# Optimization experiments

Measured on AMD Instinct MI355X. Metric: run time of the kernel, lower is better.

Reference implementation:

```python
import jax, jax.numpy as jnp
import numpy as np

EPS = 1e-6
ROPE_BASE = 10000.0
N_HEADS = 16
N_KV_HEADS = 4
NUM_EXPERTS = 8
TOP_K = 2


def rms_norm(x, w):
    rms = jax.lax.rsqrt(jnp.mean(x * x, axis=-1, keepdims=True) + EPS)
    return x * rms * w


def rope_tables(seq_len, head_dim):
    inv_freq = 1.0 / ROPE_BASE ** (jnp.arange(0, head_dim, 2, dtype=jnp.float32) / head_dim)
    t = jnp.arange(seq_len, dtype=jnp.float32)
    freqs = jnp.outer(t, inv_freq)              # [S, D/2]
    emb = jnp.concatenate([freqs, freqs], -1)    # [S, D]
    return jnp.cos(emb), jnp.sin(emb)


def apply_rotary(x, cos, sin):
    # x: [B, S, H, D]; cos/sin: [S, D]
    c = cos[None, :, None, 0::2]
    s = sin[None, :, None, 0::2]
    x1 = x[..., 0::2]
    x2 = x[..., 1::2]
    y1 = x1 * c - x2 * s
    y2 = x1 * s + x2 * c
    return jnp.stack([y1, y2], axis=-1).reshape(x.shape)


def attention(x, wq, wk, wv, wo):
    B, S, D = x.shape
    hd = D // N_HEADS
    q = (x @ wq.T).reshape(B, S, N_HEADS, hd)
    k = (x @ wk.T).reshape(B, S, N_KV_HEADS, hd)
    v = (x @ wv.T).reshape(B, S, N_KV_HEADS, hd)
    cos, sin = rope_tables(S, hd)
    q = apply_rotary(q, cos, sin)
    k = apply_rotary(k, cos, sin)
    n_rep = N_HEADS // N_KV_HEADS
    k = jnp.repeat(k, n_rep, axis=2)
    v = jnp.repeat(v, n_rep, axis=2)
    q = q.transpose(0, 2, 1, 3)  # [B,H,S,D]
    k = k.transpose(0, 2, 1, 3)
    v = v.transpose(0, 2, 1, 3)
    scores = jnp.einsum('bhqd,bhkd->bhqk', q, k) / jnp.sqrt(jnp.float32(hd))
    causal = jnp.tril(jnp.ones((S, S), dtype=bool))
    scores = jnp.where(causal[None, None], scores, jnp.finfo(scores.dtype).min)
    attn = jax.nn.softmax(scores, axis=-1)
    out = jnp.einsum('bhqk,bhkd->bhqd', attn, v)
    out = out.transpose(0, 2, 1, 3).reshape(B, S, D)
    return out @ wo.T


def moe(x, router_w, Wg, Wu, Wd):
    B, S, D = x.shape
    logits = x @ router_w.T                       # [B,S,E]
    probs = jax.nn.softmax(logits, axis=-1)
    topk_probs, topk_idx = jax.lax.top_k(probs, TOP_K)
    topk_probs = topk_probs / jnp.sum(topk_probs, axis=-1, keepdims=True)
    one_hot = jax.nn.one_hot(topk_idx, NUM_EXPERTS, dtype=jnp.float32)  # [B,S,K,E]
    tokens_per_expert = jnp.sum(one_hot, axis=(0, 1, 2))                # [E]
    f = tokens_per_expert / jnp.sum(tokens_per_expert)
    P = jnp.mean(probs.reshape(-1, NUM_EXPERTS), axis=0)
    aux_loss = NUM_EXPERTS * jnp.sum(f * P)
    # Dense all-expert SwiGLU then gather-combine (same math as masked dispatch)
    g = jnp.einsum('bsd,efd->bsef', x, Wg)        # [B,S,E,F]
    u = jnp.einsum('bsd,efd->bsef', x, Wu)
    h = jax.nn.silu(g) * u
    y = jnp.einsum('bsef,edf->bsed', h, Wd)       # [B,S,E,D]
    idx = jnp.broadcast_to(topk_idx[..., None], (B, S, TOP_K, D))
    sel = jnp.take_along_axis(y, idx, axis=2)     # [B,S,K,D]
    out = jnp.sum(topk_probs[..., None] * sel, axis=2)
    return out, aux_loss, tokens_per_expert


def setup_inputs() -> dict:
    key = jax.random.key(0)
    ks = jax.random.split(key, 9)
    d_model, d_ff, E = 1024, 2048, NUM_EXPERTS
    sc = 0.02
    return {
        'x': jax.random.normal(ks[0], (2, 2048, d_model), jnp.float32),
        'wq': jax.random.normal(ks[1], (d_model, d_model), jnp.float32) * sc,
        'wk': jax.random.normal(ks[2], (256, d_model), jnp.float32) * sc,
        'wv': jax.random.normal(ks[3], (256, d_model), jnp.float32) * sc,
        'wo': jax.random.normal(ks[4], (d_model, d_model), jnp.float32) * sc,
        'attn_norm_w': jnp.ones((d_model,), jnp.float32),
        'ffn_norm_w': jnp.ones((d_model,), jnp.float32),
        'router_w': jax.random.normal(ks[5], (E, d_model), jnp.float32) * sc,
        'Wg': jax.random.normal(ks[6], (E, d_ff, d_model), jnp.float32) * sc,
        'Wu': jax.random.normal(ks[7], (E, d_ff, d_model), jnp.float32) * sc,
        'Wd': jax.random.normal(ks[8], (E, d_model, d_ff), jnp.float32) * sc,
    }


def reference(x, wq, wk, wv, wo, attn_norm_w, ffn_norm_w, router_w, Wg, Wu, Wd):
    x = x + attention(rms_norm(x, attn_norm_w), wq, wk, wv, wo)
    moe_out, aux_loss, tokens_per_expert = moe(rms_norm(x, ffn_norm_w), router_w, Wg, Wu, Wd)
    x = x + moe_out
    return (x, aux_loss, tokens_per_expert)
```

## Files before the change

kernel.cpp:

```cpp
#include <hip/hip_runtime.h>
#include <hip/hip_bf16.h>
#include <math.h>

typedef __attribute__((ext_vector_type(4))) float f32x4;
typedef __attribute__((ext_vector_type(8))) short bf16x8;
typedef __attribute__((ext_vector_type(8))) unsigned short u16x8;

#define D_MODEL 1024
#define DFF 2048
#define S_LEN 2048
#define T_TOK 4096
#define NEXP 8

__device__ __forceinline__ unsigned short f2bf(float f){
  union { float f; unsigned u; } v; v.f = f;
  unsigned u = v.u;
  u += 0x7fffu + ((u >> 16) & 1u);
  return (unsigned short)(u >> 16);
}

__global__ __launch_bounds__(256) void k_rmsnorm(const float* __restrict__ x,
    const float* __restrict__ w, float* __restrict__ out){
  const int t = blockIdx.x;
  const int tid = threadIdx.x;
  const float* row = x + (size_t)t * D_MODEL;
  float4 v = *(const float4*)(row + tid * 4);
  float ss = v.x*v.x + v.y*v.y + v.z*v.z + v.w*v.w;
  #pragma unroll
  for (int m = 1; m < 64; m <<= 1) ss += __shfl_xor(ss, m);
  __shared__ float red[4];
  if ((tid & 63) == 0) red[tid >> 6] = ss;
  __syncthreads();
  float tot = red[0] + red[1] + red[2] + red[3];
  float mean = tot * (1.0f / D_MODEL);
  float r = (float)(1.0 / sqrt((double)mean + 1e-6));
  float4 wv = *(const float4*)(w + tid * 4);
  float4 o;
  o.x = v.x * r * wv.x; o.y = v.y * r * wv.y;
  o.z = v.z * r * wv.z; o.w = v.w * r * wv.w;
  *(float4*)(out + (size_t)t * D_MODEL + tid * 4) = o;
}

__global__ __launch_bounds__(256) void k_gemm_f32(
    const float* __restrict__ A, int lda,
    const float* __restrict__ B0, const float* __restrict__ B1, const float* __restrict__ B2,
    int nb1, int nb2,
    float* __restrict__ C, int ldc,
    const float* __restrict__ resid, int K)
{
  __shared__ float As[16][132];
  __shared__ float Bs[16][132];
  const int n0 = blockIdx.x * 128, m0 = blockIdx.y * 128;
  const float* Bp; int nsub;
  if (B2 && n0 >= nb2)      { Bp = B2; nsub = n0 - nb2; }
  else if (B1 && n0 >= nb1) { Bp = B1; nsub = n0 - nb1; }
  else                      { Bp = B0; nsub = n0; }
  const int tid = threadIdx.x;
  const int sr = tid >> 1, sc = (tid & 1) << 3;
  const float* ap = A + (size_t)(m0 + sr) * lda + sc;
  const float* bp = Bp + (size_t)(nsub + sr) * K + sc;
  float acc[8][8];
  #pragma unroll
  for (int i = 0; i < 8; i++)
    #pragma unroll
    for (int j = 0; j < 8; j++) acc[i][j] = 0.f;
  const int tm = (tid >> 4) << 3, tn = (tid & 15) << 3;
  for (int k0 = 0; k0 < K; k0 += 16){
    float4 a0 = *(const float4*)(ap + k0);
    float4 a1 = *(const float4*)(ap + k0 + 4);
    float4 b0 = *(const float4*)(bp + k0);
    float4 b1 = *(const float4*)(bp + k0 + 4);
    As[sc+0][sr] = a0.x; As[sc+1][sr] = a0.y; As[sc+2][sr] = a0.z; As[sc+3][sr] = a0.w;
    As[sc+4][sr] = a1.x; As[sc+5][sr] = a1.y; As[sc+6][sr] = a1.z; As[sc+7][sr] = a1.w;
    Bs[sc+0][sr] = b0.x; Bs[sc+1][sr] = b0.y; Bs[sc+2][sr] = b0.z; Bs[sc+3][sr] = b0.w;
    Bs[sc+4][sr] = b1.x; Bs[sc+5][sr] = b1.y; Bs[sc+6][sr] = b1.z; Bs[sc+7][sr] = b1.w;
    __syncthreads();
    #pragma unroll
    for (int kk = 0; kk < 16; kk++){
      float a[8], b[8];
      *(float4*)(a)     = *(const float4*)&As[kk][tm];
      *(float4*)(a + 4) = *(const float4*)&As[kk][tm + 4];
      *(float4*)(b)     = *(const float4*)&Bs[kk][tn];
      *(float4*)(b + 4) = *(const float4*)&Bs[kk][tn + 4];
      #pragma unroll
      for (int i = 0; i < 8; i++)
        #pragma unroll
        for (int j = 0; j < 8; j++) acc[i][j] = fmaf(a[i], b[j], acc[i][j]);
    }
    __syncthreads();
  }
  #pragma unroll
  for (int i = 0; i < 8; i++){
    int row = m0 + tm + i;
    float* cp = C + (size_t)row * ldc + n0 + tn;
    if (resid){
      const float* rp = resid + (size_t)row * ldc + n0 + tn;
      #pragma unroll
      for (int j = 0; j < 8; j++) cp[j] = acc[i][j] + rp[j];
    } else {
      float4 v0, v1;
      v0.x = acc[i][0]; v0.y = acc[i][1]; v0.z = acc[i][2]; v0.w = acc[i][3];
      v1.x = acc[i][4]; v1.y = acc[i][5]; v1.z = acc[i][6]; v1.w = acc[i][7];
      *(float4*)cp = v0; *(float4*)(cp + 4) = v1;
    }
  }
}

__global__ void k_rope_table(float* __restrict__ ctab, float* __restrict__ stab){
  int idx = blockIdx.x * 256 + threadIdx.x;
  int pos = idx >> 4, kx = idx & 15;
  double inv = 1.0 / pow(10000.0, (double)kx / 16.0);
  float invf = (float)inv;
  float ang = (float)pos * invf;
  ctab[idx] = (float)cos((double)ang);
  stab[idx] = (float)sin((double)ang);
}

__global__ __launch_bounds__(256) void k_rope(float* __restrict__ qkv,
    const float* __restrict__ ctab, const float* __restrict__ stab){
  int idx = blockIdx.x * 256 + threadIdx.x;
  int t = idx / 640, p = idx - t * 640;
  int col, ph;
  if (p < 512){ int h = p >> 5; ph = p & 31; col = h * 64 + 2 * ph; }
  else { int p2 = p - 512; int h = p2 >> 5; ph = p2 & 31; col = 1024 + h * 64 + 2 * ph; }
  int pos = t & (S_LEN - 1);
  float c = ctab[pos * 16 + (ph & 15)];
  float s = stab[pos * 16 + (ph & 15)];
  float* base = qkv + (size_t)t * 1536 + col;
  float x1 = base[0], x2 = base[1];
  base[0] = x1 * c - x2 * s;
  base[1] = x1 * s + x2 * c;
}

__global__ __launch_bounds__(64) void k_attn(float* __restrict__ qkv){
  const int bx = blockIdx.x;
  const int h  = blockIdx.y;
  const int b  = blockIdx.z;
  const int tid = threadIdx.x;
  const int tok = b * S_LEN + bx * 64 + tid;
  __shared__ float Ks[64][68];
  __shared__ float Vs[64][68];
  float q[64], O[64];
  {
    const float* qp = qkv + (size_t)tok * 1536 + h * 64;
    #pragma unroll
    for (int c = 0; c < 16; c++){
      float4 v = *(const float4*)(qp + c * 4);
      q[c*4+0] = v.x * 0.125f; q[c*4+1] = v.y * 0.125f;
      q[c*4+2] = v.z * 0.125f; q[c*4+3] = v.w * 0.125f;
    }
  }
  #pragma unroll
  for (int d = 0; d < 64; d++) O[d] = 0.f;
  float m = -INFINITY, l = 0.f;
  const int kvh = h >> 2;
  const float* kbase = qkv + (size_t)(b * S_LEN) * 1536 + 1024 + kvh * 64;
  const float* vbase = kbase + 256;
  for (int kt = 0; kt <= bx; ++kt){
    #pragma unroll
    for (int i = 0; i < 16; i++){
      int r = i * 4 + (tid >> 4);
      int c = (tid & 15) << 2;
      size_t grow = (size_t)(kt * 64 + r) * 1536;
      *(float4*)&Ks[r][c] = *(const float4*)(kbase + grow + c);
      *(float4*)&Vs[r][c] = *(const float4*)(vbase + grow + c);
    }
    __syncthreads();
    const int jmax = (kt == bx) ? tid : 63;
    #pragma unroll
    for (int ch = 0; ch < 2; ++ch){
      const int jb = ch * 32;
      float s[32];
      #pragma unroll
      for (int jj = 0; jj < 32; jj += 2){
        float s0 = 0.f, s1 = 0.f;
        const float* kr0 = &Ks[jb + jj][0];
        const float* kr1 = &Ks[jb + jj + 1][0];
        #pragma unroll
        for (int c = 0; c < 16; c++){
          float4 k0 = *(const float4*)(kr0 + c * 4);
          float4 k1 = *(const float4*)(kr1 + c * 4);
          s0 = fmaf(q[c*4+0], k0.x, s0); s0 = fmaf(q[c*4+1], k0.y, s0);
          s0 = fmaf(q[c*4+2], k0.z, s0); s0 = fmaf(q[c*4+3], k0.w, s0);
          s1 = fmaf(q[c*4+0], k1.x, s1); s1 = fmaf(q[c*4+1], k1.y, s1);
          s1 = fmaf(q[c*4+2], k1.z, s1); s1 = fmaf(q[c*4+3], k1.w, s1);
        }
        s[jj] = s0; s[jj + 1] = s1;
      }
      float tmax = -INFINITY;
      #pragma unroll
      for (int jj = 0; jj < 32; jj++)
        if (jb + jj <= jmax) tmax = fmaxf(tmax, s[jj]);
      float mn = fmaxf(m, tmax);
      float corr = expf(m - mn);
      l *= corr;
      #pragma unroll
      for (int d = 0; d < 64; d++) O[d] *= corr;
      float ps = 0.f;
      #pragma unroll
      for (int jj = 0; jj < 32; jj++){
        float p = (jb + jj <= jmax) ? expf(s[jj] - mn) : 0.f;
        s[jj] = p; ps += p;
      }
      l += ps;
      #pragma unroll
      for (int jj = 0; jj < 32; jj++){
        float p = s[jj];
        const float* vr = &Vs[jb + jj][0];
        #pragma unroll
        for (int c = 0; c < 16; c++){
          float4 v4 = *(const float4*)(vr + c * 4);
          O[c*4+0] = fmaf(p, v4.x, O[c*4+0]);
          O[c*4+1] = fmaf(p, v4.y, O[c*4+1]);
          O[c*4+2] = fmaf(p, v4.z, O[c*4+2]);
          O[c*4+3] = fmaf(p, v4.w, O[c*4+3]);
        }
      }
      m = mn;
    }
    __syncthreads();
  }
  float inv_l = 1.f / l;
  float* op = qkv + (size_t)tok * 1536 + h * 64;
  #pragma unroll
  for (int c = 0; c < 16; c++){
    float4 o4;
    o4.x = O[c*4+0] * inv_l; o4.y = O[c*4+1] * inv_l;
    o4.z = O[c*4+2] * inv_l; o4.w = O[c*4+3] * inv_l;
    *(float4*)(op + c * 4) = o4;
  }
}

__global__ __launch_bounds__(64) void k_router(const float* __restrict__ norm2,
    const float* __restrict__ rw, float* __restrict__ p_all,
    int2* __restrict__ idx2, float2* __restrict__ tokw){
  const int t = blockIdx.x;
  const int lane = threadIdx.x;
  const float* xr = norm2 + (size_t)t * D_MODEL;
  float part[8];
  #pragma unroll
  for (int e = 0; e < 8; e++) part[e] = 0.f;
  #pragma unroll
  for (int c = 0; c < 4; c++){
    float4 xv = *(const float4*)(xr + c * 256 + lane * 4);
    #pragma unroll
    for (int e = 0; e < 8; e++){
      float4 wv = *(const float4*)(rw + e * D_MODEL + c * 256 + lane * 4);
      part[e] += xv.x*wv.x + xv.y*wv.y + xv.z*wv.z + xv.w*wv.w;
    }
  }
  #pragma unroll
  for (int e = 0; e < 8; e++){
    float v = part[e];
    #pragma unroll
    for (int msk = 1; msk < 64; msk <<= 1) v += __shfl_xor(v, msk);
    part[e] = v;
  }
  if (lane == 0){
    float mx = part[0];
    #pragma unroll
    for (int e = 1; e < 8; e++) mx = fmaxf(mx, part[e]);
    float p[8]; float sum = 0.f;
    #pragma unroll
    for (int e = 0; e < 8; e++){ p[e] = expf(part[e] - mx); sum += p[e]; }
    float inv = 1.f / sum;
    #pragma unroll
    for (int e = 0; e < 8; e++) p[e] *= inv;
    int i1 = 0;
    for (int e = 1; e < 8; e++) if (p[e] > p[i1]) i1 = e;
    int i2 = (i1 == 0) ? 1 : 0;
    for (int e = 0; e < 8; e++){ if (e != i1 && p[e] > p[i2]) i2 = e; }
    float denom = p[i1] + p[i2];
    float2 w; w.x = p[i1] / denom; w.y = p[i2] / denom;
    #pragma unroll
    for (int e = 0; e < 8; e++) p_all[t * 8 + e] = p[e];
    idx2[t] = make_int2(i1, i2);
    tokw[t] = w;
  }
}

__global__ __launch_bounds__(256) void k_finalize(const float* __restrict__ p_all,
    const int2* __restrict__ idx2, float* __restrict__ out,
    int* __restrict__ cnt, int* __restrict__ offs, int* __restrict__ cursor){
  __shared__ int sc[8];
  __shared__ float sp[8];
  const int tid = threadIdx.x;
  if (tid < 8){ sc[tid] = 0; sp[tid] = 0.f; }
  __syncthreads();
  int cl[8]; float pl[8];
  #pragma unroll
  for (int e = 0; e < 8; e++){ cl[e] = 0; pl[e] = 0.f; }
  for (int t = tid; t < T_TOK; t += 256){
    int2 id = idx2[t];
    cl[id.x]++; cl[id.y]++;
    #pragma unroll
    for (int e = 0; e < 8; e++) pl[e] += p_all[t * 8 + e];
  }
  #pragma unroll
  for (int e = 0; e < 8; e++){ atomicAdd(&sc[e], cl[e]); atomicAdd(&sp[e], pl[e]); }
  __syncthreads();
  if (tid == 0){
    float aux = 0.f; int off = 0;
    for (int e = 0; e < 8; e++){
      out[4194305 + e] = (float)sc[e];
      aux += ((float)sc[e] / 8192.0f) * (sp[e] / 4096.0f);
      offs[e] = off; cnt[e] = sc[e]; cursor[e] = 0; off += sc[e];
    }
    out[4194304] = aux * 8.0f;
  }
}

__global__ __launch_bounds__(256) void k_scatter(const int2* __restrict__ idx2,
    const float2* __restrict__ tokw, const int* __restrict__ offs,
    int* __restrict__ cursor, int* __restrict__ perm, float* __restrict__ wgt){
  int t = blockIdx.x * 256 + threadIdx.x;
  if (t >= T_TOK) return;
  int2 id = idx2[t]; float2 w = tokw[t];
  int p1 = atomicAdd(&cursor[id.x], 1);
  perm[offs[id.x] + p1] = t; wgt[offs[id.x] + p1] = w.x;
  int p2 = atomicAdd(&cursor[id.y], 1);
  perm[offs[id.y] + p2] = t; wgt[offs[id.y] + p2] = w.y;
}

__global__ __launch_bounds__(256) void k_moe_a(
    const float* __restrict__ norm2, const float* __restrict__ Wg, const float* __restrict__ Wu,
    const int* __restrict__ cnt, const int* __restrict__ offs,
    const int* __restrict__ perm, unsigned short* __restrict__ Hbuf)
{
  int rem = blockIdx.x, e = -1, m0 = 0;
  #pragma unroll
  for (int i = 0; i < 8; i++){
    int nt = (cnt[i] + 63) >> 6;
    if (e < 0 && rem < nt){ e = i; m0 = rem << 6; }
    if (e < 0) rem -= nt;
  }
  if (e < 0) return;
  const int n0 = blockIdx.y * 128;
  const int ne = cnt[e];
  const int seg0 = offs[e];
  __shared__ unsigned short As[64][40];
  __shared__ unsigned short Bg[128][40];
  __shared__ unsigned short Bu[128][40];
  const int tid = threadIdx.x;
  const int lane = tid & 63, w = tid >> 6;
  const int wm = w >> 1, wn = w & 1;
  f32x4 accg[2][4], accu[2][4];
  #pragma unroll
  for (int i = 0; i < 2; i++)
    #pragma unroll
    for (int j = 0; j < 4; j++){
      accg[i][j] = (f32x4){0.f,0.f,0.f,0.f};
      accu[i][j] = (f32x4){0.f,0.f,0.f,0.f};
    }
  const int ar = tid >> 1, ah = (tid & 1) << 4;
  bool aval = false; const float* asrc = norm2;
  if (tid < 128){
    aval = (m0 + ar < ne);
    int token = aval ? perm[seg0 + m0 + ar] : 0;
    asrc = norm2 + (size_t)token * D_MODEL + ah;
  }
  const int br = tid & 127;
  const float* bsrc = ((tid >> 7) ? Wu : Wg) + (size_t)e * DFF * D_MODEL
                      + (size_t)(n0 + br) * D_MODEL;
  unsigned short (*Bt)[40] = (tid >> 7) ? Bu : Bg;
  const int fr = lane & 15, fk = (lane >> 4) << 3;
  for (int k0 = 0; k0 < D_MODEL; k0 += 32){
    if (tid < 128){
      u16x8 w0 = (u16x8){0,0,0,0,0,0,0,0}, w1 = w0;
      if (aval){
        float4 f0 = *(const float4*)(asrc + k0);
        float4 f1 = *(const float4*)(asrc + k0 + 4);
        float4 f2 = *(const float4*)(asrc + k0 + 8);
        float4 f3 = *(const float4*)(asrc + k0 + 12);
        w0[0]=f2bf(f0.x); w0[1]=f2bf(f0.y); w0[2]=f2bf(f0.z); w0[3]=f2bf(f0.w);
        w0[4]=f2bf(f1.x); w0[5]=f2bf(f1.y); w0[6]=f2bf(f1.z); w0[7]=f2bf(f1.w);
        w1[0]=f2bf(f2.x); w1[1]=f2bf(f2.y); w1[2]=f2bf(f2.z); w1[3]=f2bf(f2.w);
        w1[4]=f2bf(f3.x); w1[5]=f2bf(f3.y); w1[6]=f2bf(f3.z); w1[7]=f2bf(f3.w);
      }
      *(u16x8*)&As[ar][ah] = w0;
      *(u16x8*)&As[ar][ah + 8] = w1;
    }
    {
      float4 f0 = *(const float4*)(bsrc + k0);
      float4 f1 = *(const float4*)(bsrc + k0 + 4);
      float4 f2 = *(const float4*)(bsrc + k0 + 8);
      float4 f3 = *(const float4*)(bsrc + k0 + 12);
      float4 f4 = *(const float4*)(bsrc + k0 + 16);
      float4 f5 = *(const float4*)(bsrc + k0 + 20);
      float4 f6 = *(const float4*)(bsrc + k0 + 24);
      float4 f7 = *(const float4*)(bsrc + k0 + 28);
      u16x8 w0, w1, w2, w3;
      w0[0]=f2bf(f0.x); w0[1]=f2bf(f0.y); w0[2]=f2bf(f0.z); w0[3]=f2bf(f0.w);
      w0[4]=f2bf(f1.x); w0[5]=f2bf(f1.y); w0[6]=f2bf(f1.z); w0[7]=f2bf(f1.w);
      w1[0]=f2bf(f2.x); w1[1]=f2bf(f2.y); w1[2]=f2bf(f2.z); w1[3]=f2bf(f2.w);
      w1[4]=f2bf(f3.x); w1[5]=f2bf(f3.y); w1[6]=f2bf(f3.z); w1[7]=f2bf(f3.w);
      w2[0]=f2bf(f4.x); w2[1]=f2bf(f4.y); w2[2]=f2bf(f4.z); w2[3]=f2bf(f4.w);
      w2[4]=f2bf(f5.x); w2[5]=f2bf(f5.y); w2[6]=f2bf(f5.z); w2[7]=f2bf(f5.w);
      w3[0]=f2bf(f6.x); w3[1]=f2bf(f6.y); w3[2]=f2bf(f6.z); w3[3]=f2bf(f6.w);
      w3[4]=f2bf(f7.x); w3[5]=f2bf(f7.y); w3[6]=f2bf(f7.z); w3[7]=f2bf(f7.w);
      *(u16x8*)&Bt[br][0]  = w0; *(u16x8*)&Bt[br][8]  = w1;
      *(u16x8*)&Bt[br][16] = w2; *(u16x8*)&Bt[br][24] = w3;
    }
    __syncthreads();
    bf16x8 af0 = *(const bf16x8*)&As[wm*32 + fr][fk];
    bf16x8 af1 = *(const bf16x8*)&As[wm*32 + 16 + fr][fk];
    #pragma unroll
    for (int fn = 0; fn < 4; fn++){
      bf16x8 bg = *(const bf16x8*)&Bg[wn*64 + fn*16 + fr][fk];
      bf16x8 bu = *(const bf16x8*)&Bu[wn*64 + fn*16 + fr][fk];
      accg[0][fn] = __builtin_amdgcn_mfma_f32_16x16x32_bf16(af0, bg, accg[0][fn], 0, 0, 0);
      accg[1][fn] = __builtin_amdgcn_mfma_f32_16x16x32_bf16(af1, bg, accg[1][fn], 0, 0, 0);
      accu[0][fn] = __builtin_amdgcn_mfma_f32_16x16x32_bf16(af0, bu, accu[0][fn], 0, 0, 0);
      accu[1][fn] = __builtin_amdgcn_mfma_f32_16x16x32_bf16(af1, bu, accu[1][fn], 0, 0, 0);
    }
    __syncthreads();
  }
  const int r0 = (lane >> 4) << 2, cix = lane & 15;
  #pragma unroll
  for (int fm = 0; fm < 2; fm++)
    #pragma unroll
    for (int fn = 0; fn < 4; fn++)
      #pragma unroll
      for (int reg = 0; reg < 4; reg++){
        int ml = wm*32 + fm*16 + r0 + reg;
        if (m0 + ml < ne){
          int nl = wn*64 + fn*16 + cix;
          float g = accg[fm][fn][reg];
          float u = accu[fm][fn][reg];
          float h = g / (1.f + __expf(-g)) * u;
          Hbuf[(size_t)(seg0 + m0 + ml) * DFF + n0 + nl] = f2bf(h);
        }
      }
}

__global__ __launch_bounds__(256) void k_moe_b(
    const unsigned short* __restrict__ Hbuf, const float* __restrict__ Wd,
    const int* __restrict__ cnt, const int* __restrict__ offs,
    const int* __restrict__ perm, const float* __restrict__ wgt,
    float* __restrict__ outx)
{
  int rem = blockIdx.x, e = -1, m0 = 0;
  #pragma unroll
  for (int i = 0; i < 8; i++){
    int nt = (cnt[i] + 63) >> 6;
    if (e < 0 && rem < nt){ e = i; m0 = rem << 6; }
    if (e < 0) rem -= nt;
  }
  if (e < 0) return;
  const int n0 = blockIdx.y * 128;
  const int ne = cnt[e];
  const int seg0 = offs[e];
  __shared__ unsigned short As[64][40];
  __shared__ unsigned short Bs[128][40];
  const int tid = threadIdx.x;
  const int lane = tid & 63, w = tid >> 6;
  const int wm = w >> 1, wn = w & 1;
  f32x4 acc[2][4];
  #pragma unroll
  for (int i = 0; i < 2; i++)
    #pragma unroll
    for (int j = 0; j < 4; j++) acc[i][j] = (f32x4){0.f,0.f,0.f,0.f};
  const int ar = tid >> 1, ah = (tid & 1) << 4;
  const bool aval = (tid < 128) && (m0 + ar < ne);
  const unsigned short* asrc = aval ? (Hbuf + (size_t)(seg0 + m0 + ar) * DFF + ah) : Hbuf;
  const int br = tid >> 1, bh = (tid & 1) << 4;
  const float* bsrc = Wd + (size_t)e * D_MODEL * DFF + (size_t)(n0 + br) * DFF + bh;
  const int fr = lane & 15, fk = (lane >> 4) << 3;
  for (int k0 = 0; k0 < DFF; k0 += 32){
    if (tid < 128){
      u16x8 w0 = (u16x8){0,0,0,0,0,0,0,0}, w1 = w0;
      if (aval){
        w0 = *(const u16x8*)(asrc + k0);
        w1 = *(const u16x8*)(asrc + k0 + 8);
      }
      *(u16x8*)&As[ar][ah] = w0;
      *(u16x8*)&As[ar][ah + 8] = w1;
    }
    {
      float4 f0 = *(const float4*)(bsrc + k0);
      float4 f1 = *(const float4*)(bsrc + k0 + 4);
      float4 f2 = *(const float4*)(bsrc + k0 + 8);
      float4 f3 = *(const float4*)(bsrc + k0 + 12);
      u16x8 w0, w1;
      w0[0]=f2bf(f0.x); w0[1]=f2bf(f0.y); w0[2]=f2bf(f0.z); w0[3]=f2bf(f0.w);
      w0[4]=f2bf(f1.x); w0[5]=f2bf(f1.y); w0[6]=f2bf(f1.z); w0[7]=f2bf(f1.w);
      w1[0]=f2bf(f2.x); w1[1]=f2bf(f2.y); w1[2]=f2bf(f2.z); w1[3]=f2bf(f2.w);
      w1[4]=f2bf(f3.x); w1[5]=f2bf(f3.y); w1[6]=f2bf(f3.z); w1[7]=f2bf(f3.w);
      *(u16x8*)&Bs[br][bh] = w0;
      *(u16x8*)&Bs[br][bh + 8] = w1;
    }
    __syncthreads();
    bf16x8 af0 = *(const bf16x8*)&As[wm*32 + fr][fk];
    bf16x8 af1 = *(const bf16x8*)&As[wm*32 + 16 + fr][fk];
    #pragma unroll
    for (int fn = 0; fn < 4; fn++){
      bf16x8 bf = *(const bf16x8*)&Bs[wn*64 + fn*16 + fr][fk];
      acc[0][fn] = __builtin_amdgcn_mfma_f32_16x16x32_bf16(af0, bf, acc[0][fn], 0, 0, 0);
      acc[1][fn] = __builtin_amdgcn_mfma_f32_16x16x32_bf16(af1, bf, acc[1][fn], 0, 0, 0);
    }
    __syncthreads();
  }
  const int r0 = (lane >> 4) << 2, cix = lane & 15;
  #pragma unroll
  for (int fm = 0; fm < 2; fm++)
    #pragma unroll
    for (int reg = 0; reg < 4; reg++){
      int ml = wm*32 + fm*16 + r0 + reg;
      if (m0 + ml < ne){
        int g = seg0 + m0 + ml;
        int token = perm[g];
        float wwt = wgt[g];
        #pragma unroll
        for (int fn = 0; fn < 4; fn++){
          int nl = wn*64 + fn*16 + cix;
          atomicAdd(&outx[(size_t)token * D_MODEL + n0 + nl], wwt * acc[fm][fn][reg]);
        }
      }
    }
}

extern "C" void kernel_launch(void* const* d_in, const int* in_sizes, int n_in,
                              void* d_out, int out_size, void* d_ws, size_t ws_size,
                              hipStream_t stream)
{
  const float* x   = (const float*)d_in[0];
  const float* wq  = (const float*)d_in[1];
  const float* wk  = (const float*)d_in[2];
  const float* wv  = (const float*)d_in[3];
  const float* wo  = (const float*)d_in[4];
  const float* anw = (const float*)d_in[5];
  const float* fnw = (const float*)d_in[6];
  const float* rw  = (const float*)d_in[7];
  const float* Wg  = (const float*)d_in[8];
  const float* Wu  = (const float*)d_in[9];
  const float* Wd  = (const float*)d_in[10];
  float* out = (float*)d_out;

  char* ws = (char*)d_ws;
  size_t off = 0;
  auto alloc = [&](size_t bytes){ char* p = ws + off; off += (bytes + 255) & ~(size_t)255; return p; };
  float* norm            = (float*)alloc((size_t)T_TOK * D_MODEL * 4);
  float* qkv             = (float*)alloc((size_t)T_TOK * 1536 * 4);
  unsigned short* Hbuf   = (unsigned short*)alloc((size_t)8192 * DFF * 2);
  float* ctab            = (float*)alloc(2048 * 16 * 4);
  float* stab            = (float*)alloc(2048 * 16 * 4);
  float* p_all           = (float*)alloc((size_t)T_TOK * 8 * 4);
  int2* idx2             = (int2*)alloc((size_t)T_TOK * 8);
  float2* tokw           = (float2*)alloc((size_t)T_TOK * 8);
  int* cnt               = (int*)alloc(32);
  int* offs              = (int*)alloc(32);
  int* cursor            = (int*)alloc(32);
  int* perm              = (int*)alloc(8192 * 4);
  float* wgt             = (float*)alloc(8192 * 4);

  k_rope_table<<<128, 256, 0, stream>>>(ctab, stab);
  k_rmsnorm<<<T_TOK, 256, 0, stream>>>(x, anw, norm);
  k_gemm_f32<<<dim3(12, 32), 256, 0, stream>>>(norm, D_MODEL, wq, wk, wv, 1024, 1280,
                                               qkv, 1536, nullptr, D_MODEL);
  k_rope<<<(T_TOK * 640) / 256, 256, 0, stream>>>(qkv, ctab, stab);
  k_attn<<<dim3(32, 16, 2), 64, 0, stream>>>(qkv);
  k_gemm_f32<<<dim3(8, 32), 256, 0, stream>>>(qkv, 1536, wo, nullptr, nullptr, 1 << 29, 1 << 29,
                                              out, D_MODEL, x, D_MODEL);
  k_rmsnorm<<<T_TOK, 256, 0, stream>>>(out, fnw, norm);
  k_router<<<T_TOK, 64, 0, stream>>>(norm, rw, p_all, idx2, tokw);
  k_finalize<<<1, 256, 0, stream>>>(p_all, idx2, out, cnt, offs, cursor);
  k_scatter<<<16, 256, 0, stream>>>(idx2, tokw, offs, cursor, perm, wgt);
  k_moe_a<<<dim3(136, 16), 256, 0, stream>>>(norm, Wg, Wu, cnt, offs, perm, Hbuf);
  k_moe_b<<<dim3(136, 8), 256, 0, stream>>>(Hbuf, Wd, cnt, offs, perm, wgt, out);
}
```

Baseline: 2.997 ms.

## Split causal attention over KV chunks with a separate combine pass

Attention is split into a partial kernel that processes up to four KV chunks per query tile in parallel and writes unnormalized outputs plus running max and sum. A combine kernel then merges the partials with log-sum-exp rescaling. The aim is to balance the causal triangle and raise the number of blocks in flight, since the old grid had only 1024 blocks of 64 threads with very uneven work. The partial kernel also drops LDS tiling and reads K and V straight from global memory, and it uses fast __expf. This adds extra global traffic for the partials and one more launch, and the partial buffer is aliased over workspace that later kernels reuse.

```diff
diff --git a/kernel.cpp b/kernel.cpp
--- a/kernel.cpp
+++ b/kernel.cpp
@@ -132,102 +132,131 @@
   base[1] = x1 * s + x2 * c;
 }
 
-__global__ __launch_bounds__(64) void k_attn(float* __restrict__ qkv){
-  const int bx = blockIdx.x;
-  const int h  = blockIdx.y;
-  const int b  = blockIdx.z;
+__global__ __launch_bounds__(64) void k_attn_part(const float* __restrict__ qkv,
+    float* __restrict__ Opart, float* __restrict__ ml, int C){
+  const int bx = blockIdx.x, h = blockIdx.y;
+  const int nc_max = gridDim.z >> 1;
+  const int b = blockIdx.z / nc_max;
+  const int c = blockIdx.z - b * nc_max;
+  const int L = (bx + 1) * 64;
+  const int kv0 = c * C;
+  if (kv0 >= L) return;
+  const int kv1 = min(kv0 + C, L);
   const int tid = threadIdx.x;
-  const int tok = b * S_LEN + bx * 64 + tid;
-  __shared__ float Ks[64][68];
-  __shared__ float Vs[64][68];
-  float q[64], O[64];
-  {
-    const float* qp = qkv + (size_t)tok * 1536 + h * 64;
-    #pragma unroll
-    for (int c = 0; c < 16; c++){
-      float4 v = *(const float4*)(qp + c * 4);
-      q[c*4+0] = v.x * 0.125f; q[c*4+1] = v.y * 0.125f;
-      q[c*4+2] = v.z * 0.125f; q[c*4+3] = v.w * 0.125f;
-    }
-  }
+  const int qrow = bx * 64 + tid;
+  const float* qp = qkv + ((size_t)(b * S_LEN + qrow)) * 1536 + h * 64;
+  float q[64];
+  #pragma unroll
+  for (int d4 = 0; d4 < 16; d4++){
+    float4 v = *(const float4*)(qp + d4 * 4);
+    q[d4*4+0] = v.x * 0.125f; q[d4*4+1] = v.y * 0.125f;
+    q[d4*4+2] = v.z * 0.125f; q[d4*4+3] = v.w * 0.125f;
+  }
+  float O[64];
   #pragma unroll
   for (int d = 0; d < 64; d++) O[d] = 0.f;
   float m = -INFINITY, l = 0.f;
-  const int kvh = h >> 2;
-  const float* kbase = qkv + (size_t)(b * S_LEN) * 1536 + 1024 + kvh * 64;
-  const float* vbase = kbase + 256;
-  for (int kt = 0; kt <= bx; ++kt){
-    #pragma unroll
-    for (int i = 0; i < 16; i++){
-      int r = i * 4 + (tid >> 4);
-      int c = (tid & 15) << 2;
-      size_t grow = (size_t)(kt * 64 + r) * 1536;
-      *(float4*)&Ks[r][c] = *(const float4*)(kbase + grow + c);
-      *(float4*)&Vs[r][c] = *(const float4*)(vbase + grow + c);
-    }
-    __syncthreads();
-    const int jmax = (kt == bx) ? tid : 63;
-    #pragma unroll
-    for (int ch = 0; ch < 2; ++ch){
-      const int jb = ch * 32;
-      float s[32];
+  const float* kb = qkv + (size_t)(b * S_LEN) * 1536 + 1024 + (h >> 2) * 64;
+  const float* vb = kb + 256;
+  for (int j0 = kv0; j0 < kv1; j0 += 32){
+    float s[32];
+    #pragma unroll
+    for (int jj = 0; jj < 32; jj++){
+      const float* kr = kb + (size_t)(j0 + jj) * 1536;
+      float a0 = 0.f, a1 = 0.f;
       #pragma unroll
-      for (int jj = 0; jj < 32; jj += 2){
-        float s0 = 0.f, s1 = 0.f;
-        const float* kr0 = &Ks[jb + jj][0];
-        const float* kr1 = &Ks[jb + jj + 1][0];
-        #pragma unroll
-        for (int c = 0; c < 16; c++){
-          float4 k0 = *(const float4*)(kr0 + c * 4);
-          float4 k1 = *(const float4*)(kr1 + c * 4);
-          s0 = fmaf(q[c*4+0], k0.x, s0); s0 = fmaf(q[c*4+1], k0.y, s0);
-          s0 = fmaf(q[c*4+2], k0.z, s0); s0 = fmaf(q[c*4+3], k0.w, s0);
-          s1 = fmaf(q[c*4+0], k1.x, s1); s1 = fmaf(q[c*4+1], k1.y, s1);
-          s1 = fmaf(q[c*4+2], k1.z, s1); s1 = fmaf(q[c*4+3], k1.w, s1);
-        }
-        s[jj] = s0; s[jj + 1] = s1;
+      for (int d4 = 0; d4 < 8; d4++){
+        float4 k0 = *(const float4*)(kr + d4 * 8);
+        float4 k1 = *(const float4*)(kr + d4 * 8 + 4);
+        a0 = fmaf(q[d4*8+0], k0.x, a0); a0 = fmaf(q[d4*8+1], k0.y, a0);
+        a0 = fmaf(q[d4*8+2], k0.z, a0); a0 = fmaf(q[d4*8+3], k0.w, a0);
+        a1 = fmaf(q[d4*8+4], k1.x, a1); a1 = fmaf(q[d4*8+5], k1.y, a1);
+        a1 = fmaf(q[d4*8+6], k1.z, a1); a1 = fmaf(q[d4*8+7], k1.w, a1);
       }
-      float tmax = -INFINITY;
+      s[jj] = a0 + a1;
+    }
+    const int jm = qrow - j0;
+    float tmax = -INFINITY;
+    #pragma unroll
+    for (int jj = 0; jj < 32; jj++)
+      tmax = fmaxf(tmax, (jj <= jm) ? s[jj] : -INFINITY);
+    float mn = fmaxf(m, tmax);
+    float corr = __expf(m - mn);
+    l *= corr;
+    #pragma unroll
+    for (int d = 0; d < 64; d++) O[d] *= corr;
+    float ps = 0.f;
+    #pragma unroll
+    for (int jj = 0; jj < 32; jj++){
+      float p = (jj <= jm) ? __expf(s[jj] - mn) : 0.f;
+      s[jj] = p; ps += p;
+    }
+    l += ps;
+    #pragma unroll
+    for (int jj = 0; jj < 32; jj++){
+      const float p = s[jj];
+      const float* vr = vb + (size_t)(j0 + jj) * 1536;
       #pragma unroll
-      for (int jj = 0; jj < 32; jj++)
-        if (jb + jj <= jmax) tmax = fmaxf(tmax, s[jj]);
-      float mn = fmaxf(m, tmax);
-      float corr = expf(m - mn);
-      l *= corr;
-      #pragma unroll
-      for (int d = 0; d < 64; d++) O[d] *= corr;
-      float ps = 0.f;
-      #pragma unroll
-      for (int jj = 0; jj < 32; jj++){
-        float p = (jb + jj <= jmax) ? expf(s[jj] - mn) : 0.f;
-        s[jj] = p; ps += p;
+      for (int d4 = 0; d4 < 16; d4++){
+        float4 v4 = *(const float4*)(vr + d4 * 4);
+        O[d4*4+0] = fmaf(p, v4.x, O[d4*4+0]);
+        O[d4*4+1] = fmaf(p, v4.y, O[d4*4+1]);
+        O[d4*4+2] = fmaf(p, v4.z, O[d4*4+2]);
+        O[d4*4+3] = fmaf(p, v4.w, O[d4*4+3]);
       }
-      l += ps;
-      #pragma unroll
-      for (int jj = 0; jj < 32; jj++){
-        float p = s[jj];
-        const float* vr = &Vs[jb + jj][0];
-        #pragma unroll
-        for (int c = 0; c < 16; c++){
-          float4 v4 = *(const float4*)(vr + c * 4);
-          O[c*4+0] = fmaf(p, v4.x, O[c*4+0]);
-          O[c*4+1] = fmaf(p, v4.y, O[c*4+1]);
-          O[c*4+2] = fmaf(p, v4.z, O[c*4+2]);
-          O[c*4+3] = fmaf(p, v4.w, O[c*4+3]);
-        }
-      }
-      m = mn;
-    }
-    __syncthreads();
-  }
-  float inv_l = 1.f / l;
-  float* op = qkv + (size_t)tok * 1536 + h * 64;
-  #pragma unroll
-  for (int c = 0; c < 16; c++){
+    }
+    m = mn;
+  }
+  const int uid = ((b * nc_max + c) * 16 + h) * 32 + bx;
+  float* op = Opart + (size_t)uid * 4096;
+  #pragma unroll
+  for (int d4 = 0; d4 < 16; d4++){
     float4 o4;
-    o4.x = O[c*4+0] * inv_l; o4.y = O[c*4+1] * inv_l;
-    o4.z = O[c*4+2] * inv_l; o4.w = O[c*4+3] * inv_l;
-    *(float4*)(op + c * 4) = o4;
+    o4.x = O[d4*4+0]; o4.y = O[d4*4+1]; o4.z = O[d4*4+2]; o4.w = O[d4*4+3];
+    *(float4*)(op + d4 * 256 + tid * 4) = o4;
+  }
+  ml[(size_t)uid * 128 + tid] = m;
+  ml[(size_t)uid * 128 + 64 + tid] = l;
+}
+
+__global__ __launch_bounds__(64) void k_attn_comb(const float* __restrict__ Opart,
+    const float* __restrict__ ml, float* __restrict__ qkv, int C){
+  const int bx = blockIdx.x, h = blockIdx.y, b = blockIdx.z;
+  const int tid = threadIdx.x;
+  const int L = (bx + 1) * 64;
+  const int NC = (L + C - 1) / C;
+  const int nc_max = (S_LEN + C - 1) / C;
+  float m = -INFINITY;
+  for (int c = 0; c < NC; c++){
+    int uid = ((b * nc_max + c) * 16 + h) * 32 + bx;
+    m = fmaxf(m, ml[(size_t)uid * 128 + tid]);
+  }
+  float O[64];
+  #pragma unroll
+  for (int d = 0; d < 64; d++) O[d] = 0.f;
+  float l = 0.f;
+  for (int c = 0; c < NC; c++){
+    int uid = ((b * nc_max + c) * 16 + h) * 32 + bx;
+    float w = __expf(ml[(size_t)uid * 128 + tid] - m);
+    l = fmaf(ml[(size_t)uid * 128 + 64 + tid], w, l);
+    const float* op = Opart + (size_t)uid * 4096;
+    #pragma unroll
+    for (int d4 = 0; d4 < 16; d4++){
+      float4 v = *(const float4*)(op + d4 * 256 + tid * 4);
+      O[d4*4+0] = fmaf(w, v.x, O[d4*4+0]);
+      O[d4*4+1] = fmaf(w, v.y, O[d4*4+1]);
+      O[d4*4+2] = fmaf(w, v.z, O[d4*4+2]);
+      O[d4*4+3] = fmaf(w, v.w, O[d4*4+3]);
+    }
+  }
+  float inv = 1.f / l;
+  float* qp = qkv + ((size_t)(b * S_LEN + bx * 64 + tid)) * 1536 + h * 64;
+  #pragma unroll
+  for (int d4 = 0; d4 < 16; d4++){
+    float4 o4;
+    o4.x = O[d4*4+0] * inv; o4.y = O[d4*4+1] * inv;
+    o4.z = O[d4*4+2] * inv; o4.w = O[d4*4+3] * inv;
+    *(float4*)(qp + d4 * 4) = o4;
   }
 }
 
@@ -422,13 +451,13 @@
     for (int fn = 0; fn < 4; fn++)
       #pragma unroll
       for (int reg = 0; reg < 4; reg++){
-        int ml = wm*32 + fm*16 + r0 + reg;
-        if (m0 + ml < ne){
+        int ml2 = wm*32 + fm*16 + r0 + reg;
+        if (m0 + ml2 < ne){
           int nl = wn*64 + fn*16 + cix;
           float g = accg[fm][fn][reg];
           float u = accu[fm][fn][reg];
           float h = g / (1.f + __expf(-g)) * u;
-          Hbuf[(size_t)(seg0 + m0 + ml) * DFF + n0 + nl] = f2bf(h);
+          Hbuf[(size_t)(seg0 + m0 + ml2) * DFF + n0 + nl] = f2bf(h);
         }
       }
 }
@@ -505,9 +534,9 @@
   for (int fm = 0; fm < 2; fm++)
     #pragma unroll
     for (int reg = 0; reg < 4; reg++){
-      int ml = wm*32 + fm*16 + r0 + reg;
-      if (m0 + ml < ne){
-        int g = seg0 + m0 + ml;
+      int ml2 = wm*32 + fm*16 + r0 + reg;
+      if (m0 + ml2 < ne){
+        int g = seg0 + m0 + ml2;
         int token = perm[g];
         float wwt = wgt[g];
         #pragma unroll
@@ -539,8 +568,9 @@
   char* ws = (char*)d_ws;
   size_t off = 0;
   auto alloc = [&](size_t bytes){ char* p = ws + off; off += (bytes + 255) & ~(size_t)255; return p; };
+  float* qkv             = (float*)alloc((size_t)T_TOK * 1536 * 4);
+  size_t alias_base = off;
   float* norm            = (float*)alloc((size_t)T_TOK * D_MODEL * 4);
-  float* qkv             = (float*)alloc((size_t)T_TOK * 1536 * 4);
   unsigned short* Hbuf   = (unsigned short*)alloc((size_t)8192 * DFF * 2);
   float* ctab            = (float*)alloc(2048 * 16 * 4);
   float* stab            = (float*)alloc(2048 * 16 * 4);
@@ -553,12 +583,21 @@
   int* perm              = (int*)alloc(8192 * 4);
   float* wgt             = (float*)alloc(8192 * 4);
 
+  int nc_max = 4;
+  size_t need4 = (size_t)1024 * 4 * (4096 + 128) * 4;
+  size_t avail = (ws_size > alias_base) ? (ws_size - alias_base) : 0;
+  if (avail < need4) nc_max = 2;
+  const int C = S_LEN / nc_max;
+  float* Opart = (float*)(ws + alias_base);
+  float* mlb   = Opart + (size_t)1024 * nc_max * 4096;
+
   k_rope_table<<<128, 256, 0, stream>>>(ctab, stab);
   k_rmsnorm<<<T_TOK, 256, 0, stream>>>(x, anw, norm);
   k_gemm_f32<<<dim3(12, 32), 256, 0, stream>>>(norm, D_MODEL, wq, wk, wv, 1024, 1280,
                                                qkv, 1536, nullptr, D_MODEL);
   k_rope<<<(T_TOK * 640) / 256, 256, 0, stream>>>(qkv, ctab, stab);
-  k_attn<<<dim3(32, 16, 2), 64, 0, stream>>>(qkv);
+  k_attn_part<<<dim3(32, 16, 2 * nc_max), 64, 0, stream>>>(qkv, Opart, mlb, C);
+  k_attn_comb<<<dim3(32, 16, 2), 64, 0, stream>>>(Opart, mlb, qkv, C);
   k_gemm_f32<<<dim3(8, 32), 256, 0, stream>>>(qkv, 1536, wo, nullptr, nullptr, 1 << 29, 1 << 29,
                                               out, D_MODEL, x, D_MODEL);
   k_rmsnorm<<<T_TOK, 256, 0, stream>>>(out, fnw, norm);
```

New measurement: 2.613 ms. 1.15x faster.
